# Optimization experiments

Hardware: AMD Instinct MI355X
Metric: run time of the kernel (lower is better)

## Reference

```python
import jax, jax.numpy as jnp
import numpy as np

KEY_DIM = 1024
VALUE_DIM = 1024
NUM_HEADS = 16
ORIGIN_SHAPE = (8, 16, 16)  # T, H, W video-token grid
LOCAL_BLOCKS = 3
B = 1
S = int(np.prod(ORIGIN_SHAPE))  # 2048
DH = KEY_DIM // NUM_HEADS       # 64
DV = VALUE_DIM // NUM_HEADS


def make_layout():
    """Vectorized equivalent of SparseAttention.make_layout (causal=True)."""
    shape = np.array(ORIGIN_SHAPE, dtype=np.int64)
    cum = np.concatenate([np.flip(np.cumprod(np.flip(shape)))[1:], [1]]).astype(np.int64)
    idx = np.arange(S, dtype=np.int64)
    coords = (idx[None, :] // cum[:, None]) % shape[:, None]  # [ndim, S]
    diff = idx[:, None] - idx[None, :]
    layout = (diff >= 0) & (diff <= LOCAL_BLOCKS)  # causal local window
    for d in range(len(ORIGIN_SHAPE) - 1):  # causal axial strides along dims 0..ndim-2
        same = np.ones((S, S), dtype=bool)
        for e in range(len(ORIGIN_SHAPE)):
            if e != d:
                same &= coords[e][:, None] == coords[e][None, :]
        layout |= same & (coords[d][None, :] <= coords[d][:, None])
    return layout  # [S, S] bool


def setup_inputs() -> dict:
    key = jax.random.key(0)
    ks = jax.random.split(key, 11)
    sc = 0.02
    inp = {
        "query": jax.random.normal(ks[0], (B, S, KEY_DIM), jnp.float32),
        "key":   jax.random.normal(ks[1], (B, S, KEY_DIM), jnp.float32),
        "value": jax.random.normal(ks[2], (B, S, VALUE_DIM), jnp.float32),
        "wq": sc * jax.random.normal(ks[3], (KEY_DIM, KEY_DIM), jnp.float32),
        "bq": jnp.zeros((KEY_DIM,), jnp.float32),
        "wk": sc * jax.random.normal(ks[4], (KEY_DIM, KEY_DIM), jnp.float32),
        "bk": jnp.zeros((KEY_DIM,), jnp.float32),
        "wv": sc * jax.random.normal(ks[5], (VALUE_DIM, VALUE_DIM), jnp.float32),
        "bv": jnp.zeros((VALUE_DIM,), jnp.float32),
        "wo": sc * jax.random.normal(ks[6], (VALUE_DIM, KEY_DIM), jnp.float32),
        "bo": jnp.zeros((KEY_DIM,), jnp.float32),
        "layout": jnp.asarray(make_layout(), jnp.int32)[None, None],  # [1,1,S,S]
    }
    return inp


def reference(query, key, value, wq, bq, wk, bk, wv, bv, wo, bo, layout):
    def split(x, d):  # [B,S,H*d] -> [B,H,S,d]
        return x.reshape(B, S, NUM_HEADS, d).transpose(0, 2, 1, 3)
    q = split(query @ wq + bq, DH)
    k = split(key @ wk + bk, DH)
    v = split(value @ wv + bv, DV)
    logits = jnp.einsum('bhsd,bhtd->bhst', q, k) / jnp.sqrt(jnp.float32(DH))
    logits = jnp.where(layout > 0, logits, jnp.float32(-1e9))
    attn = jax.nn.softmax(logits, axis=-1)  # matches tf.sparse.softmax over layout support
    out = jnp.einsum('bhst,bhtd->bhsd', attn, v)
    out = out.transpose(0, 2, 1, 3).reshape(B, S, VALUE_DIM)
    return out @ wo + bo
```

## Files before the change

### kernel.cpp

```cpp
#include <hip/hip_runtime.h>
#include <hip/hip_bf16.h>
#include <cstdint>
#include <math.h>

#define SEQ    2048
#define DMODEL 1024
#define NHEAD  16
#define DHEAD  64
#define NZPAD  32

typedef __bf16 bf16;
typedef __bf16 bf16x8 __attribute__((ext_vector_type(8)));
typedef float  f32x4  __attribute__((ext_vector_type(4)));

typedef __attribute__((address_space(3))) uint32_t lds_u32;
typedef __attribute__((address_space(1))) const uint32_t global_u32;

__device__ __forceinline__ void async_load16(const void* g, void* l) {
    __builtin_amdgcn_global_load_lds((global_u32*)g, (lds_u32*)l, 16, 0, 0);
}

#define CAST_BLOCKS 3072
#define TR_BLOCKS   4096
#define NZ_BLOCKS   512

__global__ __launch_bounds__(256) void prep_kernel(
    const float* __restrict__ q, const float* __restrict__ k, const float* __restrict__ v,
    bf16* __restrict__ qx, bf16* __restrict__ kx, bf16* __restrict__ vx,
    const float* __restrict__ w0, const float* __restrict__ w1,
    const float* __restrict__ w2, const float* __restrict__ w3,
    bf16* __restrict__ t0, bf16* __restrict__ t1,
    bf16* __restrict__ t2, bf16* __restrict__ t3,
    const int* __restrict__ layout, int* __restrict__ nzidx, int* __restrict__ nzcnt) {
    __shared__ float tile[32][33];
    const int bid = blockIdx.x;
    if (bid < CAST_BLOCKS) {
        const int z = bid >> 10;
        const float* src = (z == 0) ? q : (z == 1) ? k : v;
        bf16* dst        = (z == 0) ? qx : (z == 1) ? kx : vx;
        const int i = (bid & 1023) * 256 + threadIdx.x;
        const float4* s4 = (const float4*)src;
        float4 a = s4[i * 2 + 0];
        float4 b = s4[i * 2 + 1];
        bf16x8 o;
        o[0] = (bf16)a.x; o[1] = (bf16)a.y; o[2] = (bf16)a.z; o[3] = (bf16)a.w;
        o[4] = (bf16)b.x; o[5] = (bf16)b.y; o[6] = (bf16)b.z; o[7] = (bf16)b.w;
        ((bf16x8*)dst)[i] = o;
    } else if (bid < CAST_BLOCKS + TR_BLOCKS) {
        const int b = bid - CAST_BLOCKS;
        const int z = b >> 10, rem = b & 1023;
        const float* w = (z == 0) ? w0 : (z == 1) ? w1 : (z == 2) ? w2 : w3;
        bf16* t        = (z == 0) ? t0 : (z == 1) ? t1 : (z == 2) ? t2 : t3;
        const int tx = threadIdx.x & 31, ty = threadIdx.x >> 5;
        const int kbase = (rem >> 5) * 32, nbase = (rem & 31) * 32;
#pragma unroll
        for (int i = 0; i < 4; ++i)
            tile[ty + 8 * i][tx] = w[(size_t)(kbase + ty + 8 * i) * DMODEL + nbase + tx];
        __syncthreads();
#pragma unroll
        for (int i = 0; i < 4; ++i)
            t[(size_t)(nbase + ty + 8 * i) * DMODEL + kbase + tx] = (bf16)tile[tx][ty + 8 * i];
    } else {
        const int b = bid - CAST_BLOCKS - TR_BLOCKS;
        const int wv = threadIdx.x >> 6, lane = threadIdx.x & 63;
        const int s = b * 4 + wv;
        const int* row = layout + (size_t)s * SEQ;
        int base = 0;
        for (int it = 0; it < SEQ / 64; ++it) {
            const int col = it * 64 + lane;
            const bool nz = row[col] > 0;
            const unsigned long long mask = __ballot(nz);
            if (nz) {
                const int pos = base + __popcll(mask & ((1ull << lane) - 1ull));
                if (pos < NZPAD) nzidx[s * NZPAD + pos] = col;
            }
            base += __popcll(mask);
        }
        const int cnt = (base < NZPAD) ? base : NZPAD;
        if (lane >= cnt && lane < NZPAD) nzidx[s * NZPAD + lane] = s;
        if (lane == 0) nzcnt[s] = cnt;
    }
}

template <int TM, typename OutT>
__device__ __forceinline__ void gemm_bt_body(
    const bf16* __restrict__ A, const bf16* __restrict__ BT,
    const float* __restrict__ bias, OutT* __restrict__ C) {
    constexpr int K = 1024, N = 1024;
    constexpr int MI  = TM / 32;
    constexpr int ACH = TM * 4;
    __shared__ bf16 sA[TM * 32];
    __shared__ bf16 sB[128 * 32];
    const int tid = threadIdx.x;
    const int w = tid >> 6, lane = tid & 63;
    const int wm = w >> 1, wn = w & 1;
    const int lr = lane & 15, quad = lane >> 4;
    const int m0 = blockIdx.y * TM, n0 = blockIdx.x * 128;

    f32x4 acc[MI][4] = {};
    float bia[4];
#pragma unroll
    for (int ni = 0; ni < 4; ++ni) bia[ni] = bias[n0 + wn * 64 + ni * 16 + lr];

    for (int kt = 0; kt < K; kt += 32) {
#pragma unroll
        for (int kk = 0; kk < (ACH + 512) / 256; ++kk) {
            const int cb = kk * 256 + w * 64;
            const int c  = cb + lane;
            if (cb < ACH) {
                const int row = c >> 2, ch = c & 3;
                async_load16(A + (size_t)(m0 + row) * K + kt + ch * 8,
                             (char*)sA + cb * 16);
            } else {
                const int c2 = c - ACH, row = c2 >> 2, ch = c2 & 3;
                async_load16(BT + (size_t)(n0 + row) * K + kt + ch * 8,
                             (char*)sB + (cb - ACH) * 16);
            }
        }
        __syncthreads();

        bf16x8 af[MI], bfr[4];
#pragma unroll
        for (int mi = 0; mi < MI; ++mi)
            af[mi] = *(const bf16x8*)&sA[(wm * (TM / 2) + mi * 16 + lr) * 32 + quad * 8];
#pragma unroll
        for (int ni = 0; ni < 4; ++ni)
            bfr[ni] = *(const bf16x8*)&sB[(wn * 64 + ni * 16 + lr) * 32 + quad * 8];
#pragma unroll
        for (int mi = 0; mi < MI; ++mi)
#pragma unroll
            for (int ni = 0; ni < 4; ++ni)
                acc[mi][ni] = __builtin_amdgcn_mfma_f32_16x16x32_bf16(
                    af[mi], bfr[ni], acc[mi][ni], 0, 0, 0);
        __syncthreads();
    }

#pragma unroll
    for (int mi = 0; mi < MI; ++mi)
#pragma unroll
        for (int ni = 0; ni < 4; ++ni) {
            const int row = m0 + wm * (TM / 2) + mi * 16 + quad * 4;
            const int col = n0 + wn * 64 + ni * 16 + lr;
            const f32x4 vv = acc[mi][ni];
#pragma unroll
            for (int r = 0; r < 4; ++r)
                C[(size_t)(row + r) * N + col] = (OutT)(vv[r] + bia[ni]);
        }
}

__global__ __launch_bounds__(256) void proj3_kernel(
    const bf16* qx, const bf16* kx, const bf16* vx,
    const bf16* wqT, const bf16* wkT, const bf16* wvT,
    const float* bq, const float* bk, const float* bv,
    bf16* qp, bf16* kp, bf16* vp) {
    const int z = blockIdx.z;
    const bf16* A  = (z == 0) ? qx : (z == 1) ? kx : vx;
    const bf16* BT = (z == 0) ? wqT : (z == 1) ? wkT : wvT;
    const float* b = (z == 0) ? bq : (z == 1) ? bk : bv;
    bf16* C        = (z == 0) ? qp : (z == 1) ? kp : vp;
    gemm_bt_body<64, bf16>(A, BT, b, C);
}

__global__ __launch_bounds__(256) void gemm_final_kernel(
    const bf16* A, const bf16* BT, const float* bias, float* C) {
    gemm_bt_body<64, float>(A, BT, bias, C);
}

__global__ __launch_bounds__(256) void attn_kernel(
    const bf16* __restrict__ qp, const bf16* __restrict__ kp, const bf16* __restrict__ vp,
    const int* __restrict__ nzidx, const int* __restrict__ nzcnt,
    bf16* __restrict__ ao) {
    const int wv = threadIdx.x >> 6, lane = threadIdx.x & 63;
    const int p = blockIdx.x * 4 + wv;
    const int s = __builtin_amdgcn_readfirstlane(p & (SEQ - 1));
    const int h = __builtin_amdgcn_readfirstlane(p >> 11);
    const int hbase = h * DHEAD;
    const int hoff = hbase + lane;

    const int cnt = nzcnt[s];
    const int* idx = nzidx + s * NZPAD;
    int t[NZPAD];
#pragma unroll
    for (int c = 0; c < NZPAD; ++c) t[c] = idx[c];

    const int c_lane = lane & 31;
    const int fo = (lane >> 5) << 5;
    const int myT = idx[c_lane];

    const bf16x8* qrow = (const bf16x8*)(qp + (size_t)s * DMODEL + hbase + fo);
    const bf16x8* krow = (const bf16x8*)(kp + (size_t)myT * DMODEL + hbase + fo);
    bf16x8 qc[4], kc[4];
#pragma unroll
    for (int j = 0; j < 4; ++j) { qc[j] = qrow[j]; kc[j] = krow[j]; }

    float vvv[NZPAD];
#pragma unroll
    for (int c = 0; c < NZPAD; ++c)
        vvv[c] = (float)vp[(size_t)t[c] * DMODEL + hoff];

    float dot = 0.f;
#pragma unroll
    for (int j = 0; j < 4; ++j)
#pragma unroll
        for (int e = 0; e < 8; ++e)
            dot = fmaf((float)qc[j][e], (float)kc[j][e], dot);
    dot += __shfl_xor(dot, 32);

    const float logit = (c_lane < cnt) ? dot * 0.125f : -1e30f;
    float m = logit;
    m = fmaxf(m, __shfl_xor(m, 1)); m = fmaxf(m, __shfl_xor(m, 2));
    m = fmaxf(m, __shfl_xor(m, 4)); m = fmaxf(m, __shfl_xor(m, 8));
    m = fmaxf(m, __shfl_xor(m, 16));
    const float e = __expf(logit - m);
    float ssum = e;
    ssum += __shfl_xor(ssum, 1); ssum += __shfl_xor(ssum, 2);
    ssum += __shfl_xor(ssum, 4); ssum += __shfl_xor(ssum, 8);
    ssum += __shfl_xor(ssum, 16);
    const float prob = e / ssum;

    float acc = 0.f;
#pragma unroll
    for (int c = 0; c < NZPAD; ++c) {
        const float pc = __uint_as_float(
            __builtin_amdgcn_readlane(__float_as_uint(prob), c));
        acc = fmaf(pc, vvv[c], acc);
    }
    ao[(size_t)s * DMODEL + hoff] = (bf16)acc;
}

extern "C" void kernel_launch(void* const* d_in, const int* in_sizes, int n_in,
                              void* d_out, int out_size, void* d_ws, size_t ws_size,
                              hipStream_t stream) {
    const float* query = (const float*)d_in[0];
    const float* key   = (const float*)d_in[1];
    const float* value = (const float*)d_in[2];
    const float* wq = (const float*)d_in[3];
    const float* bq = (const float*)d_in[4];
    const float* wk = (const float*)d_in[5];
    const float* bk = (const float*)d_in[6];
    const float* wv = (const float*)d_in[7];
    const float* bv = (const float*)d_in[8];
    const float* wo = (const float*)d_in[9];
    const float* bo = (const float*)d_in[10];
    const int* layout = (const int*)d_in[11];
    float* out = (float*)d_out;

    char* ws = (char*)d_ws;
    auto alloc = [&](size_t bytes) {
        char* p = ws;
        ws += (bytes + 255) & ~(size_t)255;
        return p;
    };
    bf16* qx  = (bf16*)alloc((size_t)SEQ * DMODEL * 2);
    bf16* kx  = (bf16*)alloc((size_t)SEQ * DMODEL * 2);
    bf16* vx  = (bf16*)alloc((size_t)SEQ * DMODEL * 2);
    bf16* wqT = (bf16*)alloc((size_t)DMODEL * DMODEL * 2);
    bf16* wkT = (bf16*)alloc((size_t)DMODEL * DMODEL * 2);
    bf16* wvT = (bf16*)alloc((size_t)DMODEL * DMODEL * 2);
    bf16* woT = (bf16*)alloc((size_t)DMODEL * DMODEL * 2);
    bf16* qp  = (bf16*)alloc((size_t)SEQ * DMODEL * 2);
    bf16* kp  = (bf16*)alloc((size_t)SEQ * DMODEL * 2);
    bf16* vp  = (bf16*)alloc((size_t)SEQ * DMODEL * 2);
    bf16* ao  = (bf16*)alloc((size_t)SEQ * DMODEL * 2);
    int* nzidx = (int*)alloc((size_t)SEQ * NZPAD * 4);
    int* nzcnt = (int*)alloc((size_t)SEQ * 4);

    prep_kernel<<<dim3(CAST_BLOCKS + TR_BLOCKS + NZ_BLOCKS), 256, 0, stream>>>(
        query, key, value, qx, kx, vx,
        wq, wk, wv, wo, wqT, wkT, wvT, woT,
        layout, nzidx, nzcnt);
    proj3_kernel<<<dim3(8, 32, 3), 256, 0, stream>>>(
        qx, kx, vx, wqT, wkT, wvT, bq, bk, bv, qp, kp, vp);
    attn_kernel<<<dim3(NHEAD * SEQ / 4), 256, 0, stream>>>(qp, kp, vp, nzidx, nzcnt, ao);
    gemm_final_kernel<<<dim3(8, 32), 256, 0, stream>>>(ao, woT, bo, out);
}
```

Measured before the change: 184.9 us.

## Double-buffer GEMM LDS tiles with BK=64, XOR swizzle, and remap attention blocks

The shared GEMM body now uses a K-tile of 64 with two LDS buffers, so the async global-to-LDS loads for the next tile overlap the MFMA work on the current one. It also drops one of the two barriers per iteration. LDS chunks are XOR-swizzled by row to avoid bank conflicts on the 128-byte row stride. The attention kernel remaps block IDs so consecutive hardware blocks are spread across eight groups, presumably to balance work or cache locality across XCDs. The cost is doubled LDS use, which may lower occupancy.

```diff
diff --git a/kernel.cpp b/kernel.cpp
--- a/kernel.cpp
+++ b/kernel.cpp
@@ -87,10 +87,13 @@
     const bf16* __restrict__ A, const bf16* __restrict__ BT,
     const float* __restrict__ bias, OutT* __restrict__ C) {
     constexpr int K = 1024, N = 1024;
-    constexpr int MI  = TM / 32;
-    constexpr int ACH = TM * 4;
-    __shared__ bf16 sA[TM * 32];
-    __shared__ bf16 sB[128 * 32];
+    constexpr int BK = 64;
+    constexpr int MI = TM / 32;
+    constexpr int ACH = TM * (BK / 8);
+    constexpr int BCH = 128 * (BK / 8);
+    constexpr int TCH = ACH + BCH;
+    __shared__ bf16 sA[2][TM * BK];
+    __shared__ bf16 sB[2][128 * BK];
     const int tid = threadIdx.x;
     const int w = tid >> 6, lane = tid & 63;
     const int wm = w >> 1, wn = w & 1;
@@ -102,37 +105,54 @@
 #pragma unroll
     for (int ni = 0; ni < 4; ++ni) bia[ni] = bias[n0 + wn * 64 + ni * 16 + lr];
 
-    for (int kt = 0; kt < K; kt += 32) {
-#pragma unroll
-        for (int kk = 0; kk < (ACH + 512) / 256; ++kk) {
+    auto stage = [&](int buf, int kt) {
+#pragma unroll
+        for (int kk = 0; kk < TCH / 256; ++kk) {
             const int cb = kk * 256 + w * 64;
-            const int c  = cb + lane;
+            const int p  = cb + lane;
             if (cb < ACH) {
-                const int row = c >> 2, ch = c & 3;
-                async_load16(A + (size_t)(m0 + row) * K + kt + ch * 8,
-                             (char*)sA + cb * 16);
+                const int row = p >> 3, chl = p & 7;
+                const int chg = chl ^ (row & 7);
+                async_load16(A + (size_t)(m0 + row) * K + kt + chg * 8,
+                             (char*)&sA[buf][0] + cb * 16);
             } else {
-                const int c2 = c - ACH, row = c2 >> 2, ch = c2 & 3;
-                async_load16(BT + (size_t)(n0 + row) * K + kt + ch * 8,
-                             (char*)sB + (cb - ACH) * 16);
-            }
+                const int p2 = p - ACH, row = p2 >> 3, chl = p2 & 7;
+                const int chg = chl ^ (row & 7);
+                async_load16(BT + (size_t)(n0 + row) * K + kt + chg * 8,
+                             (char*)&sB[buf][0] + (cb - ACH) * 16);
+            }
+        }
+    };
+
+    stage(0, 0);
+    __syncthreads();
+    int cur = 0;
+    for (int kt = 0; kt < K; kt += BK) {
+        if (kt + BK < K) stage(cur ^ 1, kt + BK);
+#pragma unroll
+        for (int ks = 0; ks < 2; ++ks) {
+            bf16x8 af[MI], bfr[4];
+#pragma unroll
+            for (int mi = 0; mi < MI; ++mi) {
+                const int row = wm * (TM / 2) + mi * 16 + lr;
+                af[mi] = *(const bf16x8*)
+                    &sA[cur][row * BK + ((ks * 4 + quad) ^ (row & 7)) * 8];
+            }
+#pragma unroll
+            for (int ni = 0; ni < 4; ++ni) {
+                const int row = wn * 64 + ni * 16 + lr;
+                bfr[ni] = *(const bf16x8*)
+                    &sB[cur][row * BK + ((ks * 4 + quad) ^ (row & 7)) * 8];
+            }
+#pragma unroll
+            for (int mi = 0; mi < MI; ++mi)
+#pragma unroll
+                for (int ni = 0; ni < 4; ++ni)
+                    acc[mi][ni] = __builtin_amdgcn_mfma_f32_16x16x32_bf16(
+                        af[mi], bfr[ni], acc[mi][ni], 0, 0, 0);
         }
         __syncthreads();
-
-        bf16x8 af[MI], bfr[4];
-#pragma unroll
-        for (int mi = 0; mi < MI; ++mi)
-            af[mi] = *(const bf16x8*)&sA[(wm * (TM / 2) + mi * 16 + lr) * 32 + quad * 8];
-#pragma unroll
-        for (int ni = 0; ni < 4; ++ni)
-            bfr[ni] = *(const bf16x8*)&sB[(wn * 64 + ni * 16 + lr) * 32 + quad * 8];
-#pragma unroll
-        for (int mi = 0; mi < MI; ++mi)
-#pragma unroll
-            for (int ni = 0; ni < 4; ++ni)
-                acc[mi][ni] = __builtin_amdgcn_mfma_f32_16x16x32_bf16(
-                    af[mi], bfr[ni], acc[mi][ni], 0, 0, 0);
-        __syncthreads();
+        cur ^= 1;
     }
 
 #pragma unroll
@@ -171,7 +191,9 @@
     const int* __restrict__ nzidx, const int* __restrict__ nzcnt,
     bf16* __restrict__ ao) {
     const int wv = threadIdx.x >> 6, lane = threadIdx.x & 63;
-    const int p = blockIdx.x * 4 + wv;
+    constexpr int NB = NHEAD * SEQ / 4;
+    const int bid = (blockIdx.x & 7) * (NB >> 3) + (blockIdx.x >> 3);
+    const int p = bid * 4 + wv;
     const int s = __builtin_amdgcn_readfirstlane(p & (SEQ - 1));
     const int h = __builtin_amdgcn_readfirstlane(p >> 11);
     const int hbase = h * DHEAD;
```

Measured after the change: 171.2 us. 1.08x faster.
